# Kernel tuning notes

Hardware: AMD Instinct MI355X
Metric: run time of the kernel (lower is better)

Reference implementation:

```python
import jax, jax.numpy as jnp
import numpy as np

NEG = -1000000.0  # mask fill value used by the torch module


def setup_inputs() -> dict:
    key = jax.random.key(0)
    kq, kk, kv, km = jax.random.split(key, 4)
    B, Q, K, D = 8, 2048, 2048, 128
    queries = jax.random.normal(kq, (B, Q, D), dtype=jnp.float32)
    keys = jax.random.normal(kk, (B, K, D), dtype=jnp.float32)
    values = jax.random.normal(kv, (B, K, D), dtype=jnp.float32)
    attntion_mask = jax.random.randint(km, (B, K), 0, 2, dtype=jnp.int32)
    return {"queries": queries, "keys": keys, "values": values,
            "attntion_mask": attntion_mask}


def reference(queries, keys, values, attntion_mask):
    d = queries.shape[-1]
    # scores: [B, Q, K]
    scores = jnp.einsum('bqd,bkd->bqk', queries, keys) / jnp.sqrt(
        jnp.asarray(d, dtype=queries.dtype))
    # 2D mask [B, K] broadcasts over the query axis (torch repeat_interleave)
    mask = attntion_mask.astype(bool)[:, None, :]  # [B, 1, K]
    scores = jnp.where(mask, scores, NEG)
    weights = jax.nn.softmax(scores, axis=-1)
    # dropout rate is 0.0 (eval mode) -> identity
    return jnp.einsum('bqk,bkv->bqv', weights, values)
```

## Files before the change

kernel.cpp:

```cpp
#include <hip/hip_runtime.h>
#include <stdint.h>

typedef __attribute__((ext_vector_type(8))) short short8;
typedef __attribute__((ext_vector_type(4))) float f32x4;

#define NB 8
#define NQ 2048
#define NK 2048
#define ND 128
#define SCALE 0.08838834764831845f
#define L2E   1.4426950408889634f
#define FMAXC 10.0f

__device__ __forceinline__ uint32_t pk_bf16(float a, float b) {
  uint32_t ua = __builtin_bit_cast(uint32_t, a);
  uint32_t ub = __builtin_bit_cast(uint32_t, b);
  ua += 0x7FFFu + ((ua >> 16) & 1u);
  ub += 0x7FFFu + ((ub >> 16) & 1u);
  return (ua >> 16) | (ub & 0xFFFF0000u);
}

__device__ __forceinline__ void dma16(const void* g, void* l) {
  __builtin_amdgcn_global_load_lds((const __attribute__((address_space(1))) void*)g,
                                   (__attribute__((address_space(3))) void*)l, 16, 0, 0);
}

__global__ __launch_bounds__(256) void prep_kernel(const float* __restrict__ v,
                                                   const float* __restrict__ kin,
                                                   ushort* __restrict__ vt,
                                                   ushort* __restrict__ kb) {
  const int t = threadIdx.x;
  const int bid = blockIdx.x;
  if (bid < 512) {
    __shared__ __align__(16) float tile[4096];
    char* sm = (char*)tile;
    const int b = bid >> 6;
    const int k0 = ((bid >> 1) & 31) << 6;
    const int d0 = (bid & 1) << 6;
#pragma unroll
    for (int i = 0; i < 4; ++i) {
      int id = i * 256 + t;
      int k = id >> 4, c = id & 15;
      uint4 val = *(const uint4*)(v + (size_t)(b * NK + k0 + k) * ND + d0 + c * 4);
      *(uint4*)(sm + k * 256 + ((c ^ (k & 15)) * 16)) = val;
    }
    __syncthreads();
#pragma unroll
    for (int i = 0; i < 2; ++i) {
      int id = i * 256 + t;
      int d = id >> 3, kc = id & 7;
      uint32_t w[4];
#pragma unroll
      for (int jj = 0; jj < 4; ++jj) {
        int kA = kc * 8 + jj * 2, kB = kA + 1;
        float fa = *(const float*)(sm + kA * 256 + (((d >> 2) ^ (kA & 15)) * 16) + (d & 3) * 4);
        float fb = *(const float*)(sm + kB * 256 + (((d >> 2) ^ (kB & 15)) * 16) + (d & 3) * 4);
        w[jj] = pk_bf16(fa, fb);
      }
      uint4 o; o.x = w[0]; o.y = w[1]; o.z = w[2]; o.w = w[3];
      *(uint4*)(vt + (size_t)(b * ND + d0 + d) * NK + k0 + kc * 8) = o;
    }
  } else {
    int idx = (bid - 512) * 2048 + t * 8;
    f32x4 a = *(const f32x4*)(kin + idx);
    f32x4 c = *(const f32x4*)(kin + idx + 4);
    uint4 u;
    u.x = pk_bf16(a[0], a[1]); u.y = pk_bf16(a[2], a[3]);
    u.z = pk_bf16(c[0], c[1]); u.w = pk_bf16(c[2], c[3]);
    *(uint4*)(kb + idx) = u;
  }
}

#define LDS_BYTES 73728
__global__ __launch_bounds__(256) void attn_kernel(const float* __restrict__ qm,
                                                   const ushort* __restrict__ kbm,
                                                   const ushort* __restrict__ vtm,
                                                   const int* __restrict__ maskm,
                                                   ushort* __restrict__ opart,
                                                   float* __restrict__ lpart) {
  __shared__ __align__(16) char sm[LDS_BYTES];
  const int bid = blockIdx.x;
  const int b   = bid >> 6;
  const int q0  = ((bid >> 1) & 31) << 6;
  const int spl = bid & 1;
  const int kb0 = spl << 10;
  const int t = threadIdx.x;
  const int lane = t & 63;
  const int wave = t >> 6;
  const int r = lane & 15;
  const int quad = lane >> 4;
  const int half = wave >> 1;
  const int qg = wave & 1;

  uint32_t koff[4], voff[4];
#pragma unroll
  for (int j = 0; j < 4; ++j) {
    int i = wave * 4 + j;
    int rho = i * 4 + (lane >> 4);
    int ck = (lane & 15) ^ (rho & 15);
    int krow = kb0 + (rho >> 5) * 512 + (rho & 31);
    koff[j] = (uint32_t)(b * NK + krow) * ND + ck * 8;
    int rv = i * 16 + (lane >> 2);
    int cv = (lane & 3) ^ (rv & 3);
    voff[j] = (uint32_t)(b * ND + (rv & 127)) * NK + kb0 + (rv >> 7) * 512 + cv * 8;
  }

  short8 qf[2][4];
#pragma unroll
  for (int qt = 0; qt < 2; ++qt)
#pragma unroll
    for (int ks = 0; ks < 4; ++ks) {
      const float* p = qm + (size_t)(b * NQ + q0 + qg * 32 + qt * 16 + r) * ND + ks * 32 + quad * 8;
      f32x4 a = *(const f32x4*)p;
      f32x4 c = *(const f32x4*)(p + 4);
      uint4 u;
      u.x = pk_bf16(a[0], a[1]); u.y = pk_bf16(a[2], a[3]);
      u.z = pk_bf16(c[0], c[1]); u.w = pk_bf16(c[2], c[3]);
      qf[qt][ks] = __builtin_bit_cast(short8, u);
    }

  f32x4 oacc[2][8];
#pragma unroll
  for (int qt = 0; qt < 2; ++qt)
#pragma unroll
    for (int dt = 0; dt < 8; ++dt) oacc[qt][dt] = (f32x4){0.f, 0.f, 0.f, 0.f};
  float l_[2] = {0.f, 0.f};

  char* const pbase = sm + 65536 + wave * 2048;

#pragma unroll
  for (int j = 0; j < 4; ++j) {
    dma16(kbm + koff[j], sm + wave * 4096 + j * 1024);
    dma16(vtm + voff[j], sm + 32768 + wave * 4096 + j * 1024);
  }

  for (int it = 0; it < 16; ++it) {
    const int cur = it & 1;
    char* const kcur = sm + cur * 16384;
    char* const vcur = sm + 32768 + cur * 16384;
    char* const knxt = sm + (cur ^ 1) * 16384;
    char* const vnxt = sm + 32768 + (cur ^ 1) * 16384;

    __syncthreads();

    int4 mv0 = *(const int4*)(maskm + b * NK + kb0 + half * 512 + it * 32 + quad * 4);
    int4 mv1 = *(const int4*)(maskm + b * NK + kb0 + half * 512 + it * 32 + 16 + quad * 4);

    if (it < 15) {
      const uint32_t kadd = (uint32_t)(it + 1) * 32 * ND;
      const uint32_t vadd = (uint32_t)(it + 1) * 32;
#pragma unroll
      for (int j = 0; j < 4; ++j) {
        dma16(kbm + koff[j] + kadd, knxt + wave * 4096 + j * 1024);
        dma16(vtm + voff[j] + vadd, vnxt + wave * 4096 + j * 1024);
      }
    }

    short8 kf[2][4];
#pragma unroll
    for (int mt = 0; mt < 2; ++mt)
#pragma unroll
      for (int ks = 0; ks < 4; ++ks)
        kf[mt][ks] = *(const short8*)(kcur + half * 8192 + (mt * 16 + r) * 256 + (((ks * 4 + quad) ^ r) * 16));
    f32x4 st[2][2];
#pragma unroll
    for (int mt = 0; mt < 2; ++mt)
#pragma unroll
      for (int qt = 0; qt < 2; ++qt) {
        f32x4 acc = (f32x4){0.f, 0.f, 0.f, 0.f};
#pragma unroll
        for (int ks = 0; ks < 4; ++ks)
          acc = __builtin_amdgcn_mfma_f32_16x16x32_bf16(kf[mt][ks], qf[qt][ks], acc, 0, 0, 0);
        st[mt][qt] = acc;
      }

    const float C1 = SCALE * L2E;
    const float C2 = -FMAXC * L2E;
#pragma unroll
    for (int qt = 0; qt < 2; ++qt) {
      float p[2][4]; float ps = 0.f;
#pragma unroll
      for (int mt = 0; mt < 2; ++mt) {
        const int4 mv = mt ? mv1 : mv0;
        float t0 = mv.x ? fmaf(st[mt][qt][0], C1, C2) : -2.0e6f;
        float t1 = mv.y ? fmaf(st[mt][qt][1], C1, C2) : -2.0e6f;
        float t2 = mv.z ? fmaf(st[mt][qt][2], C1, C2) : -2.0e6f;
        float t3 = mv.w ? fmaf(st[mt][qt][3], C1, C2) : -2.0e6f;
        p[mt][0] = exp2f(t0); p[mt][1] = exp2f(t1);
        p[mt][2] = exp2f(t2); p[mt][3] = exp2f(t3);
        ps += p[mt][0] + p[mt][1] + p[mt][2] + p[mt][3];
      }
      ps += __shfl_xor(ps, 16);
      ps += __shfl_xor(ps, 32);
      l_[qt] += ps;
#pragma unroll
      for (int mt = 0; mt < 2; ++mt) {
        uint2 w; w.x = pk_bf16(p[mt][0], p[mt][1]); w.y = pk_bf16(p[mt][2], p[mt][3]);
        *(uint2*)(pbase + (qt * 16 + r) * 64 + (((mt * 4 + quad) ^ (r & 6)) * 8)) = w;
      }
    }

    short8 pf[2];
#pragma unroll
    for (int qt = 0; qt < 2; ++qt)
      pf[qt] = *(const short8*)(pbase + (qt * 16 + r) * 64 + (((quad * 2) ^ (r & 6)) * 8));
#pragma unroll
    for (int dt = 0; dt < 8; ++dt) {
      short8 vf = *(const short8*)(vcur + half * 8192 + (dt * 16 + r) * 64 + ((quad ^ (r & 3)) * 16));
#pragma unroll
      for (int qt = 0; qt < 2; ++qt)
        oacc[qt][dt] = __builtin_amdgcn_mfma_f32_16x16x32_bf16(vf, pf[qt], oacc[qt][dt], 0, 0, 0);
    }
  }

  __syncthreads();
  float* xch = (float*)(sm + qg * 17408) + lane * 68;
  if (half == 1) {
    xch[0] = l_[0]; xch[1] = l_[1];
#pragma unroll
    for (int qt = 0; qt < 2; ++qt)
#pragma unroll
      for (int dt = 0; dt < 8; ++dt)
        *(f32x4*)(xch + 4 + (qt * 8 + dt) * 4) = oacc[qt][dt];
  }
  __syncthreads();
  if (half == 0) {
#pragma unroll
    for (int qt = 0; qt < 2; ++qt) {
      const int qrow = b * NQ + q0 + qg * 32 + qt * 16 + r;
      float lsum = l_[qt] + xch[qt];
      if (quad == 0) lpart[spl * NB * NQ + qrow] = lsum;
#pragma unroll
      for (int dt = 0; dt < 8; ++dt) {
        f32x4 o1 = *(const f32x4*)(xch + 4 + (qt * 8 + dt) * 4);
        f32x4 o = oacc[qt][dt] + o1;
        uint2 w; w.x = pk_bf16(o[0], o[1]); w.y = pk_bf16(o[2], o[3]);
        *(uint2*)(opart + (size_t)spl * NB * NQ * ND + (size_t)qrow * ND + dt * 16 + quad * 4) = w;
      }
    }
  }
}

__global__ __launch_bounds__(256) void merge_kernel(const ushort* __restrict__ opart,
                                                    const float* __restrict__ lpart,
                                                    float* __restrict__ outm) {
  const int gid = blockIdx.x * 256 + threadIdx.x;
  const int row = gid >> 4;
  const int d0 = (gid & 15) << 3;
  const size_t off = (size_t)row * ND + d0;
  uint4 u0 = *(const uint4*)(opart + off);
  uint4 u1 = *(const uint4*)(opart + (size_t)NB * NQ * ND + off);
  float inv = 1.0f / (lpart[row] + lpart[NB * NQ + row]);
  f32x4 lo, hi;
  uint32_t w;
#define UP(u, dst0, dst1) w = (u); dst0 = __builtin_bit_cast(float, w << 16); \
                          dst1 = __builtin_bit_cast(float, w & 0xFFFF0000u);
  float a0,a1,b0,b1;
  UP(u0.x, a0, a1) UP(u1.x, b0, b1) lo[0] = (a0 + b0) * inv; lo[1] = (a1 + b1) * inv;
  UP(u0.y, a0, a1) UP(u1.y, b0, b1) lo[2] = (a0 + b0) * inv; lo[3] = (a1 + b1) * inv;
  UP(u0.z, a0, a1) UP(u1.z, b0, b1) hi[0] = (a0 + b0) * inv; hi[1] = (a1 + b1) * inv;
  UP(u0.w, a0, a1) UP(u1.w, b0, b1) hi[2] = (a0 + b0) * inv; hi[3] = (a1 + b1) * inv;
#undef UP
  *(f32x4*)(outm + off) = lo;
  *(f32x4*)(outm + off + 4) = hi;
}

extern "C" void kernel_launch(void* const* d_in, const int* in_sizes, int n_in,
                              void* d_out, int out_size, void* d_ws, size_t ws_size,
                              hipStream_t stream) {
  const float* q   = (const float*)d_in[0];
  const float* k   = (const float*)d_in[1];
  const float* v   = (const float*)d_in[2];
  const int*   msk = (const int*)d_in[3];
  float* out = (float*)d_out;
  ushort* kb = (ushort*)d_ws;
  ushort* vt = kb + (size_t)NB * NK * ND;
  ushort* op = vt + (size_t)NB * NK * ND;
  float*  lp = (float*)(op + 2 * (size_t)NB * NQ * ND);

  prep_kernel<<<1536, 256, 0, stream>>>(v, k, vt, kb);
  attn_kernel<<<512, 256, 0, stream>>>(q, kb, vt, msk, op, lp);
  merge_kernel<<<1024, 256, 0, stream>>>(op, lp, out);
}
```

Before: 118.0 us.

## Compact unmasked keys per batch and skip masked key blocks in attention

A new compaction kernel builds, for each batch, a list of the unmasked key indices and their count. The prep kernel gathers only those K and V rows into the bf16 workspaces, zero-filling the tail. The attention kernel then loops only over the compacted length, split across the four chunks, and masks by position instead of reading the mask array. This removes the QK, softmax and PV work on masked keys, roughly half of them for this input, at the cost of an extra small kernel launch and gathered loads. A batch with no unmasked keys would give zero loop iterations and a divide by zero, where the reference returns a uniform average of V. The attention grid order is also remapped to interleave batches.

```diff
diff --git a/kernel.cpp b/kernel.cpp
--- a/kernel.cpp
+++ b/kernel.cpp
@@ -25,10 +25,38 @@
                                    (__attribute__((address_space(3))) void*)l, 16, 0, 0);
 }
 
+__global__ __launch_bounds__(256) void compact_kernel(const int* __restrict__ maskm,
+                                                      int* __restrict__ idxArr,
+                                                      int* __restrict__ KcArr) {
+  __shared__ int cnt;
+  const int b = blockIdx.x;
+  const int t = threadIdx.x;
+  const int lane = t & 63;
+  if (t == 0) cnt = 0;
+  __syncthreads();
+#pragma unroll
+  for (int j = 0; j < 8; ++j) {
+    int k = t * 8 + j;
+    bool bit = maskm[b * NK + k] != 0;
+    unsigned long long m = __ballot(bit);
+    int pre = __popcll(m & ((1ull << lane) - 1ull));
+    int tot = __popcll(m);
+    int base = 0;
+    if (lane == 0 && tot) base = atomicAdd(&cnt, tot);
+    base = __shfl(base, 0);
+    if (bit) idxArr[b * NK + base + pre] = k;
+  }
+  __syncthreads();
+  int kc = cnt;
+  for (int s = kc + t; s < NK; s += 256) idxArr[b * NK + s] = -1;
+  if (t == 0) KcArr[b] = kc;
+}
+
 __global__ __launch_bounds__(256) void prep_kernel(const float* __restrict__ v,
                                                    const float* __restrict__ kin,
                                                    ushort* __restrict__ vt,
-                                                   ushort* __restrict__ kb) {
+                                                   ushort* __restrict__ kb,
+                                                   const int* __restrict__ idxArr) {
   const int t = threadIdx.x;
   const int bid = blockIdx.x;
   if (bid < 512) {
@@ -41,7 +69,9 @@
     for (int i = 0; i < 4; ++i) {
       int id = i * 256 + t;
       int k = id >> 4, c = id & 15;
-      uint4 val = *(const uint4*)(v + (size_t)(b * NK + k0 + k) * ND + d0 + c * 4);
+      int src = idxArr[b * NK + k0 + k];
+      uint4 val; val.x = 0u; val.y = 0u; val.z = 0u; val.w = 0u;
+      if (src >= 0) val = *(const uint4*)(v + (size_t)(b * NK + src) * ND + d0 + c * 4);
       *(uint4*)(sm + k * 256 + ((c ^ (k & 15)) * 16)) = val;
     }
     __syncthreads();
@@ -61,13 +91,19 @@
       *(uint4*)(vt + (size_t)(b * ND + d0 + d) * NK + k0 + kc * 8) = o;
     }
   } else {
-    int idx = (bid - 512) * 2048 + t * 8;
-    f32x4 a = *(const f32x4*)(kin + idx);
-    f32x4 c = *(const f32x4*)(kin + idx + 4);
-    uint4 u;
-    u.x = pk_bf16(a[0], a[1]); u.y = pk_bf16(a[2], a[3]);
-    u.z = pk_bf16(c[0], c[1]); u.w = pk_bf16(c[2], c[3]);
-    *(uint4*)(kb + idx) = u;
+    int gs = (bid - 512) * 16 + (t >> 4);
+    int src = idxArr[gs];
+    int col = (t & 15) * 8;
+    uint4 u; u.x = 0u; u.y = 0u; u.z = 0u; u.w = 0u;
+    if (src >= 0) {
+      int b2 = gs >> 11;
+      const float* p = kin + (size_t)(b2 * NK + src) * ND + col;
+      f32x4 a = *(const f32x4*)p;
+      f32x4 c = *(const f32x4*)(p + 4);
+      u.x = pk_bf16(a[0], a[1]); u.y = pk_bf16(a[2], a[3]);
+      u.z = pk_bf16(c[0], c[1]); u.w = pk_bf16(c[2], c[3]);
+    }
+    *(uint4*)(kb + (size_t)gs * ND + col) = u;
   }
 }
 
@@ -75,15 +111,15 @@
 __global__ __launch_bounds__(256) void attn_kernel(const float* __restrict__ qm,
                                                    const ushort* __restrict__ kbm,
                                                    const ushort* __restrict__ vtm,
-                                                   const int* __restrict__ maskm,
+                                                   const int* __restrict__ KcArr,
                                                    ushort* __restrict__ opart,
                                                    float* __restrict__ lpart) {
   __shared__ __align__(16) char sm[LDS_BYTES];
-  const int bid = blockIdx.x;
+  const int o   = blockIdx.x;
+  const int bid = (o & 7) * 64 + (o >> 3);
   const int b   = bid >> 6;
   const int q0  = ((bid >> 1) & 31) << 6;
   const int spl = bid & 1;
-  const int kb0 = spl << 10;
   const int t = threadIdx.x;
   const int lane = t & 63;
   const int wave = t >> 6;
@@ -92,17 +128,21 @@
   const int half = wave >> 1;
   const int qg = wave & 1;
 
+  const int Kc   = KcArr[b];
+  const int n_it = (Kc + 127) >> 7;
+  const int CH   = n_it << 5;
+
   uint32_t koff[4], voff[4];
 #pragma unroll
   for (int j = 0; j < 4; ++j) {
     int i = wave * 4 + j;
     int rho = i * 4 + (lane >> 4);
     int ck = (lane & 15) ^ (rho & 15);
-    int krow = kb0 + (rho >> 5) * 512 + (rho & 31);
+    int krow = (spl * 2 + (rho >> 5)) * CH + (rho & 31);
     koff[j] = (uint32_t)(b * NK + krow) * ND + ck * 8;
     int rv = i * 16 + (lane >> 2);
     int cv = (lane & 3) ^ (rv & 3);
-    voff[j] = (uint32_t)(b * ND + (rv & 127)) * NK + kb0 + (rv >> 7) * 512 + cv * 8;
+    voff[j] = (uint32_t)(b * ND + (rv & 127)) * NK + (spl * 2 + (rv >> 7)) * CH + cv * 8;
   }
 
   short8 qf[2][4];
@@ -128,13 +168,15 @@
 
   char* const pbase = sm + 65536 + wave * 2048;
 
+  const int lim0 = Kc - (spl * 2 + half) * CH - quad * 4;
+
 #pragma unroll
   for (int j = 0; j < 4; ++j) {
     dma16(kbm + koff[j], sm + wave * 4096 + j * 1024);
     dma16(vtm + voff[j], sm + 32768 + wave * 4096 + j * 1024);
   }
 
-  for (int it = 0; it < 16; ++it) {
+  for (int it = 0; it < n_it; ++it) {
     const int cur = it & 1;
     char* const kcur = sm + cur * 16384;
     char* const vcur = sm + 32768 + cur * 16384;
@@ -143,10 +185,7 @@
 
     __syncthreads();
 
-    int4 mv0 = *(const int4*)(maskm + b * NK + kb0 + half * 512 + it * 32 + quad * 4);
-    int4 mv1 = *(const int4*)(maskm + b * NK + kb0 + half * 512 + it * 32 + 16 + quad * 4);
-
-    if (it < 15) {
+    if (it < n_it - 1) {
       const uint32_t kadd = (uint32_t)(it + 1) * 32 * ND;
       const uint32_t vadd = (uint32_t)(it + 1) * 32;
 #pragma unroll
@@ -176,16 +215,17 @@
 
     const float C1 = SCALE * L2E;
     const float C2 = -FMAXC * L2E;
+    const int rem = lim0 - it * 32;
 #pragma unroll
     for (int qt = 0; qt < 2; ++qt) {
       float p[2][4]; float ps = 0.f;
 #pragma unroll
       for (int mt = 0; mt < 2; ++mt) {
-        const int4 mv = mt ? mv1 : mv0;
-        float t0 = mv.x ? fmaf(st[mt][qt][0], C1, C2) : -2.0e6f;
-        float t1 = mv.y ? fmaf(st[mt][qt][1], C1, C2) : -2.0e6f;
-        float t2 = mv.z ? fmaf(st[mt][qt][2], C1, C2) : -2.0e6f;
-        float t3 = mv.w ? fmaf(st[mt][qt][3], C1, C2) : -2.0e6f;
+        const int rm = rem - mt * 16;
+        float t0 = (rm > 0) ? fmaf(st[mt][qt][0], C1, C2) : -2.0e6f;
+        float t1 = (rm > 1) ? fmaf(st[mt][qt][1], C1, C2) : -2.0e6f;
+        float t2 = (rm > 2) ? fmaf(st[mt][qt][2], C1, C2) : -2.0e6f;
+        float t3 = (rm > 3) ? fmaf(st[mt][qt][3], C1, C2) : -2.0e6f;
         p[mt][0] = exp2f(t0); p[mt][1] = exp2f(t1);
         p[mt][2] = exp2f(t2); p[mt][3] = exp2f(t3);
         ps += p[mt][0] + p[mt][1] + p[mt][2] + p[mt][3];
@@ -233,8 +273,8 @@
 #pragma unroll
       for (int dt = 0; dt < 8; ++dt) {
         f32x4 o1 = *(const f32x4*)(xch + 4 + (qt * 8 + dt) * 4);
-        f32x4 o = oacc[qt][dt] + o1;
-        uint2 w; w.x = pk_bf16(o[0], o[1]); w.y = pk_bf16(o[2], o[3]);
+        f32x4 ov = oacc[qt][dt] + o1;
+        uint2 w; w.x = pk_bf16(ov[0], ov[1]); w.y = pk_bf16(ov[2], ov[3]);
         *(uint2*)(opart + (size_t)spl * NB * NQ * ND + (size_t)qrow * ND + dt * 16 + quad * 4) = w;
       }
     }
@@ -277,8 +317,11 @@
   ushort* vt = kb + (size_t)NB * NK * ND;
   ushort* op = vt + (size_t)NB * NK * ND;
   float*  lp = (float*)(op + 2 * (size_t)NB * NQ * ND);
-
-  prep_kernel<<<1536, 256, 0, stream>>>(v, k, vt, kb);
-  attn_kernel<<<512, 256, 0, stream>>>(q, kb, vt, msk, op, lp);
+  int* idxA  = (int*)(lp + 2 * (size_t)NB * NQ);
+  int* kcA   = idxA + (size_t)NB * NK;
+
+  compact_kernel<<<NB, 256, 0, stream>>>(msk, idxA, kcA);
+  prep_kernel<<<1536, 256, 0, stream>>>(v, k, vt, kb, idxA);
+  attn_kernel<<<512, 256, 0, stream>>>(q, kb, vt, kcA, op, lp);
   merge_kernel<<<1024, 256, 0, stream>>>(op, lp, out);
 }
```

Measured after the change: 109.6 us. -7.2%, faster.
